# Optimization experiments

Measured on AMD Instinct MI355X. Metric: run time of the kernel, lower is better.

The kernel has to match this reference:

```python
import jax, jax.numpy as jnp
import numpy as np

B, T, D, H, L = 2, 1024, 1024, 16, 4
HD = D // H            # head_dim = 64
DFF = 4096             # 4 * d_model
VOCAB = 16384          # max_vocab_size (tied head)
MAX_CHAR = 8192        # max_char_len for RoPE table
EPS = 1e-6


def setup_inputs() -> dict:
    key = jax.random.key(0)
    ks = jax.random.split(key, 12)
    s = 0.02
    return {
        "token_ids": jax.random.randint(ks[0], (B, T), 0, 259, dtype=jnp.int32),
        "position_ids": jnp.sort(jax.random.randint(ks[1], (B, T), 0, MAX_CHAR, dtype=jnp.int32), axis=-1),
        "embed": jax.random.normal(ks[2], (VOCAB, D), jnp.float32) * s,
        "attn_norm_w": jnp.ones((L, D), jnp.float32),
        "wq": jax.random.normal(ks[3], (L, D, D), jnp.float32) * s,
        "wk": jax.random.normal(ks[4], (L, D, D), jnp.float32) * s,
        "wv": jax.random.normal(ks[5], (L, D, D), jnp.float32) * s,
        "wo": jax.random.normal(ks[6], (L, D, D), jnp.float32) * s,
        "ff_norm_w": jnp.ones((L, D), jnp.float32),
        "w1": jax.random.normal(ks[7], (L, DFF, D), jnp.float32) * s,
        "w2": jax.random.normal(ks[8], (L, D, DFF), jnp.float32) * s,
        "w3": jax.random.normal(ks[9], (L, DFF, D), jnp.float32) * s,
        "norm_w": jnp.ones((D,), jnp.float32),
    }


def _rmsnorm(x, w):
    return x * jax.lax.rsqrt(jnp.mean(x * x, axis=-1, keepdims=True) + EPS) * w


def _rope_tables():
    # precompute_freqs_cis: angles[t, i] = t / theta^(2i/dim)
    inv = 1.0 / (10000.0 ** (jnp.arange(0, HD, 2, dtype=jnp.float32) / HD))  # [HD/2]
    ang = jnp.arange(MAX_CHAR, dtype=jnp.float32)[:, None] * inv[None, :]    # [MAX_CHAR, HD/2]
    return jnp.cos(ang), jnp.sin(ang)


def _apply_rope(x, cos, sin):
    # x: [B,T,H,HD]; cos/sin: [B,T,1,HD/2] (complex multiply on (even,odd) pairs)
    xp = x.reshape(B, T, H, HD // 2, 2)
    xr, xi = xp[..., 0], xp[..., 1]
    out = jnp.stack([xr * cos - xi * sin, xr * sin + xi * cos], axis=-1)
    return out.reshape(B, T, H, HD)


def reference(token_ids, position_ids, embed, attn_norm_w, wq, wk, wv, wo,
              ff_norm_w, w1, w2, w3, norm_w):
    cos_tab, sin_tab = _rope_tables()
    cos = cos_tab[position_ids][:, :, None, :]  # [B,T,1,HD/2]
    sin = sin_tab[position_ids][:, :, None, :]

    x = embed[token_ids]  # [B,T,D] (no ghost tokens active)
    scale = 1.0 / np.sqrt(HD)

    for l in range(L):
        # --- attention block ---
        h = _rmsnorm(x, attn_norm_w[l])
        q = jnp.einsum('btd,od->bto', h, wq[l]).reshape(B, T, H, HD)
        k = jnp.einsum('btd,od->bto', h, wk[l]).reshape(B, T, H, HD)
        v = jnp.einsum('btd,od->bto', h, wv[l]).reshape(B, T, H, HD)
        q = _apply_rope(q, cos, sin)
        k = _apply_rope(k, cos, sin)
        attn = jnp.einsum('bthd,bshd->bhts', q, k) * scale  # no mask in model forward
        attn = jax.nn.softmax(attn, axis=-1)
        o = jnp.einsum('bhts,bshd->bthd', attn, v).reshape(B, T, D)
        x = x + jnp.einsum('btd,od->bto', o, wo[l])
        # --- SwiGLU FFN ---
        h = _rmsnorm(x, ff_norm_w[l])
        g = jax.nn.silu(jnp.einsum('btd,fd->btf', h, w1[l])) * jnp.einsum('btd,fd->btf', h, w3[l])
        x = x + jnp.einsum('btf,df->btd', g, w2[l])

    x = _rmsnorm(x, norm_w)
    return jnp.einsum('btd,vd->btv', x, embed)  # tied LM head -> [B,T,VOCAB]
```

## Files before the change

kernel.cpp:

```cpp
#include <hip/hip_runtime.h>

#define NTOK 2048
#define DMODEL 1024
#define NHEADS 16
#define HD_ 64
#define TSEQ 1024
#define DFF_ 4096
#define NVOCAB 16384

typedef unsigned short u16;
typedef unsigned int u32;
typedef __bf16 bf16x8 __attribute__((ext_vector_type(8)));
typedef float floatx4 __attribute__((ext_vector_type(4)));

__device__ __forceinline__ u16 f2bf(float f) {
  u32 u = __float_as_uint(f);
  u += 0x7FFFu + ((u >> 16) & 1u);
  return (u16)(u >> 16);
}
__device__ __forceinline__ float bf2f(u16 h) {
  return __uint_as_float(((u32)h) << 16);
}

__device__ __forceinline__ void gload_lds16(const void* g, void* l) {
  __builtin_amdgcn_global_load_lds(
      (const __attribute__((address_space(1))) void*)g,
      (__attribute__((address_space(3))) void*)l, 16, 0, 0);
}

__global__ void convert_bf16(const float* __restrict__ src, u16* __restrict__ dst, int n4) {
  int i = blockIdx.x * blockDim.x + threadIdx.x;
  int stride = gridDim.x * blockDim.x;
  for (; i < n4; i += stride) {
    float4 v = ((const float4*)src)[i];
    ushort4 o;
    o.x = f2bf(v.x); o.y = f2bf(v.y); o.z = f2bf(v.z); o.w = f2bf(v.w);
    ((ushort4*)dst)[i] = o;
  }
}

__global__ void convert_layer(const float* __restrict__ wq, const float* __restrict__ wk,
                              const float* __restrict__ wv, const float* __restrict__ wo,
                              const float* __restrict__ w1, const float* __restrict__ w3,
                              const float* __restrict__ w2,
                              u16* __restrict__ wqkv, u16* __restrict__ wo_b,
                              u16* __restrict__ w13, u16* __restrict__ w2_b) {
  int i = blockIdx.x * blockDim.x + threadIdx.x;
  int stride = gridDim.x * blockDim.x;
  for (; i < 4194304; i += stride) {
    const float* s; u16* d; int j;
    if (i < 262144)       { s = wq; d = wqkv;           j = i; }
    else if (i < 524288)  { s = wk; d = wqkv + 1048576; j = i - 262144; }
    else if (i < 786432)  { s = wv; d = wqkv + 2097152; j = i - 524288; }
    else if (i < 1048576) { s = wo; d = wo_b;           j = i - 786432; }
    else if (i < 2097152) { s = w1; d = w13;            j = i - 1048576; }
    else if (i < 3145728) { s = w3; d = w13 + 4194304;  j = i - 2097152; }
    else                  { s = w2; d = w2_b;           j = i - 3145728; }
    float4 v = ((const float4*)s)[j];
    ushort4 o;
    o.x = f2bf(v.x); o.y = f2bf(v.y); o.z = f2bf(v.z); o.w = f2bf(v.w);
    ((ushort4*)d)[j] = o;
  }
}

__global__ void gather_embed(const int* __restrict__ tok, const float* __restrict__ embed,
                             float* __restrict__ x) {
  int m = blockIdx.x;
  int t = tok[m];
  float4 v = ((const float4*)(embed + (long)t * DMODEL))[threadIdx.x];
  ((float4*)(x + (long)m * DMODEL))[threadIdx.x] = v;
}

__global__ void rmsnorm_bf16(const float* __restrict__ x, const float* __restrict__ w,
                             u16* __restrict__ out) {
  __shared__ float red[9];
  int m = blockIdx.x;
  int tid = threadIdx.x, lane = tid & 63, wave = tid >> 6;
  float4 v = ((const float4*)(x + (long)m * DMODEL))[tid];
  float ss = v.x * v.x + v.y * v.y + v.z * v.z + v.w * v.w;
  for (int o2 = 32; o2 > 0; o2 >>= 1) ss += __shfl_down(ss, o2);
  if (lane == 0) red[wave] = ss;
  __syncthreads();
  if (tid == 0) red[8] = rsqrtf((red[0] + red[1] + red[2] + red[3]) * (1.0f / 1024.0f) + 1e-6f);
  __syncthreads();
  float inv = red[8];
  float4 wv = ((const float4*)w)[tid];
  ushort4 o;
  o.x = f2bf(v.x * inv * wv.x); o.y = f2bf(v.y * inv * wv.y);
  o.z = f2bf(v.z * inv * wv.z); o.w = f2bf(v.w * inv * wv.w);
  ((ushort4*)(out + (long)m * DMODEL))[tid] = o;
}

__global__ void rope_qk(u16* __restrict__ qkv, const int* __restrict__ pos_ids) {
  __shared__ float cs[32], sn[32];
  int m = blockIdx.x;
  int tid = threadIdx.x;
  if (tid < 32) {
    float inv = expf(-(float)tid * (9.210340371976184f / 32.0f));
    float ang = (float)pos_ids[m] * inv;
    float s, c;
    sincosf(ang, &s, &c);
    cs[tid] = c; sn[tid] = s;
  }
  __syncthreads();
  u16* row = qkv + (long)m * 3072;
  for (int part = 0; part < 2; part++) {
    u16* base = row + part * 1024;
    for (int pp = tid; pp < 512; pp += 256) {
      int i = pp & 31;
      u32* p = (u32*)(base + pp * 2);
      u32 v = *p;
      float xr = bf2f((u16)(v & 0xFFFF));
      float xi = bf2f((u16)(v >> 16));
      float c = cs[i], s = sn[i];
      float orr = xr * c - xi * s;
      float oii = xr * s + xi * c;
      *p = (u32)f2bf(orr) | ((u32)f2bf(oii) << 16);
    }
  }
}

__global__ void transpose_v(const u16* __restrict__ qkv, u16* __restrict__ vT) {
  __shared__ u16 tile[64][65];
  int tb = blockIdx.x;
  int bh = blockIdx.y;
  int b = bh >> 4, h = bh & 15;
  const u16* src = qkv + ((long)(b * TSEQ + tb * 64)) * 3072 + 2048 + h * 64;
  for (int i = 0; i < 16; i++) {
    int e = threadIdx.x + i * 256;
    int t = e >> 6, d = e & 63;
    tile[t][d] = src[(long)t * 3072 + d];
  }
  __syncthreads();
  u16* dst = vT + ((long)bh * 64) * TSEQ + tb * 64;
  for (int i = 0; i < 16; i++) {
    int e = threadIdx.x + i * 256;
    int d = e >> 6, t = e & 63;
    dst[(long)d * TSEQ + t] = tile[t][d];
  }
}

__global__ void softmax_rows(u16* __restrict__ S) {
  __shared__ float red[9];
  long row = blockIdx.x;
  u16* p = S + row * 1024;
  int tid = threadIdx.x, lane = tid & 63, wave = tid >> 6;
  ushort4 v4 = ((const ushort4*)p)[tid];
  float v0 = bf2f(v4.x), v1 = bf2f(v4.y), v2 = bf2f(v4.z), v3 = bf2f(v4.w);
  float mx = fmaxf(fmaxf(v0, v1), fmaxf(v2, v3));
  for (int o2 = 32; o2 > 0; o2 >>= 1) mx = fmaxf(mx, __shfl_down(mx, o2));
  if (lane == 0) red[wave] = mx;
  __syncthreads();
  if (tid == 0) red[8] = fmaxf(fmaxf(red[0], red[1]), fmaxf(red[2], red[3]));
  __syncthreads();
  mx = red[8];
  float e0 = __expf(v0 - mx), e1 = __expf(v1 - mx), e2 = __expf(v2 - mx), e3 = __expf(v3 - mx);
  float s = e0 + e1 + e2 + e3;
  for (int o2 = 32; o2 > 0; o2 >>= 1) s += __shfl_down(s, o2);
  if (lane == 0) red[wave] = s;
  __syncthreads();
  if (tid == 0) red[8] = red[0] + red[1] + red[2] + red[3];
  __syncthreads();
  float inv = 1.0f / red[8];
  ushort4 o;
  o.x = f2bf(e0 * inv); o.y = f2bf(e1 * inv); o.z = f2bf(e2 * inv); o.w = f2bf(e3 * inv);
  ((ushort4*)p)[tid] = o;
}

__global__ void swiglu(const u16* __restrict__ t13, u16* __restrict__ g) {
  int i = blockIdx.x * 256 + threadIdx.x;
  int m = i >> 9, f8 = i & 511;
  const ushort4* pa = (const ushort4*)(t13 + (long)m * 8192 + f8 * 8);
  const ushort4* pb = (const ushort4*)(t13 + (long)m * 8192 + 4096 + f8 * 8);
  ushort4 a0 = pa[0], a1 = pa[1];
  ushort4 b0 = pb[0], b1 = pb[1];
  ushort4 o0, o1;
  float a, b;
#define SWG(av, bv, ov) \
  a = bf2f(av); b = bf2f(bv); ov = f2bf(a * b / (1.0f + __expf(-a)));
  SWG(a0.x, b0.x, o0.x) SWG(a0.y, b0.y, o0.y) SWG(a0.z, b0.z, o0.z) SWG(a0.w, b0.w, o0.w)
  SWG(a1.x, b1.x, o1.x) SWG(a1.y, b1.y, o1.y) SWG(a1.z, b1.z, o1.z) SWG(a1.w, b1.w, o1.w)
#undef SWG
  ushort4* po = (ushort4*)(g + (long)m * 4096 + f8 * 8);
  po[0] = o0; po[1] = o1;
}

template <int BM, int BN, int WR, int WC>
__global__ __launch_bounds__(WR * WC * 64) void gemm_nt(
    const u16* __restrict__ A, int lda, long a_sb, long a_sh,
    const u16* __restrict__ B, int ldb, long b_sb, long b_sh,
    void* __restrict__ C, int ldc, long c_sb, long c_sh,
    int K, float scale, int mode) {
  constexpr int NW = WR * WC;
  constexpr int NTHR = NW * 64;
  constexpr int WTM = BM / WR;
  constexpr int WTN = BN / WC;
  constexpr int MT = WTM / 16;
  constexpr int NT = WTN / 16;
  constexpr int ISA = (BM * 64) / (NTHR * 16);
  constexpr int ISB = (BN * 64) / (NTHR * 16);
  static_assert(ISA >= 1 && ISB >= 1, "tile too small");

  __shared__ __align__(16) u16 lA[BM * 32];
  __shared__ __align__(16) u16 lB[BN * 32];

  const int tid = threadIdx.x;
  const int lane = tid & 63;
  const int wave = tid >> 6;
  const int wm = wave / WC;
  const int wn = wave % WC;
  const int m0 = blockIdx.y * BM;
  const int n0 = blockIdx.x * BN;
  const int zb = blockIdx.z >> 4;
  const int zh = blockIdx.z & 15;
  A += (long)zb * a_sb + (long)zh * a_sh;
  B += (long)zb * b_sb + (long)zh * b_sh;
  const long c0 = (long)zb * c_sb + (long)zh * c_sh;

  floatx4 acc[MT][NT];
  for (int mi = 0; mi < MT; mi++)
    for (int ni = 0; ni < NT; ni++)
      for (int r = 0; r < 4; r++) acc[mi][ni][r] = 0.0f;

  const int q_ = lane >> 4;

  for (int k0 = 0; k0 < K; k0 += 32) {
    const u16* Ag = A + (long)m0 * lda + k0;
#pragma unroll
    for (int i = 0; i < ISA; i++) {
      int e = (tid + i * NTHR) * 8;
      int r = e >> 5;
      int c = (e >> 3) & 3;
      int csw = c ^ ((r >> 1) & 3);
      gload_lds16(Ag + (long)r * lda + (csw << 3), &lA[e]);
    }
    const u16* Bg = B + (long)n0 * ldb + k0;
#pragma unroll
    for (int i = 0; i < ISB; i++) {
      int e = (tid + i * NTHR) * 8;
      int r = e >> 5;
      int c = (e >> 3) & 3;
      int csw = c ^ ((r >> 1) & 3);
      gload_lds16(Bg + (long)r * ldb + (csw << 3), &lB[e]);
    }
    __syncthreads();

    bf16x8 af[MT], bfr[NT];
#pragma unroll
    for (int mi = 0; mi < MT; mi++) {
      int r = wm * WTM + mi * 16 + (lane & 15);
      af[mi] = *(const bf16x8*)&lA[(r << 5) + ((q_ ^ ((r >> 1) & 3)) << 3)];
    }
#pragma unroll
    for (int ni = 0; ni < NT; ni++) {
      int r = wn * WTN + ni * 16 + (lane & 15);
      bfr[ni] = *(const bf16x8*)&lB[(r << 5) + ((q_ ^ ((r >> 1) & 3)) << 3)];
    }
#pragma unroll
    for (int mi = 0; mi < MT; mi++)
#pragma unroll
      for (int ni = 0; ni < NT; ni++)
        acc[mi][ni] = __builtin_amdgcn_mfma_f32_16x16x32_bf16(af[mi], bfr[ni], acc[mi][ni], 0, 0, 0);
    __syncthreads();
  }

#pragma unroll
  for (int mi = 0; mi < MT; mi++) {
#pragma unroll
    for (int ni = 0; ni < NT; ni++) {
      int col = n0 + wn * WTN + ni * 16 + (lane & 15);
      int rbase = m0 + wm * WTM + mi * 16 + (lane >> 4) * 4;
#pragma unroll
      for (int r = 0; r < 4; r++) {
        float v = acc[mi][ni][r] * scale;
        long idx = c0 + (long)(rbase + r) * ldc + col;
        if (mode == 0)       ((float*)C)[idx] = v;
        else if (mode == 1)  ((u16*)C)[idx] = f2bf(v);
        else                 ((float*)C)[idx] += v;
      }
    }
  }
}

extern "C" void kernel_launch(void* const* d_in, const int* in_sizes, int n_in,
                              void* d_out, int out_size, void* d_ws, size_t ws_size,
                              hipStream_t stream) {
  const int*   tok         = (const int*)d_in[0];
  const int*   pos         = (const int*)d_in[1];
  const float* embed       = (const float*)d_in[2];
  const float* attn_norm_w = (const float*)d_in[3];
  const float* wq          = (const float*)d_in[4];
  const float* wk          = (const float*)d_in[5];
  const float* wv          = (const float*)d_in[6];
  const float* wo          = (const float*)d_in[7];
  const float* ff_norm_w   = (const float*)d_in[8];
  const float* w1          = (const float*)d_in[9];
  const float* w2          = (const float*)d_in[10];
  const float* w3          = (const float*)d_in[11];
  const float* norm_w      = (const float*)d_in[12];

  char* ws = (char*)d_ws;
  u16*   ebf  = (u16*)(ws);
  u16*   wqkv = (u16*)(ws + 33554432);
  u16*   wo_b = (u16*)(ws + 39845888);
  u16*   w13  = (u16*)(ws + 41943040);
  u16*   w2_b = (u16*)(ws + 58720256);
  float* x    = (float*)(ws + 67108864);
  u16*   h    = (u16*)(ws + 75497472);
  u16*   qkv  = (u16*)(ws + 79691776);
  u16*   vT   = (u16*)(ws + 92274688);
  u16*   o    = (u16*)(ws + 96468992);
  u16*   S    = (u16*)(ws + 100663296);
  u16*   t13  = S;
  u16*   g    = (u16*)(ws + 134217728);

  convert_bf16<<<16384, 256, 0, stream>>>(embed, ebf, NVOCAB * DMODEL / 4);
  gather_embed<<<NTOK, 256, 0, stream>>>(tok, embed, x);

  for (int l = 0; l < 4; l++) {
    convert_layer<<<16384, 256, 0, stream>>>(
        wq + (long)l * 1048576, wk + (long)l * 1048576, wv + (long)l * 1048576,
        wo + (long)l * 1048576, w1 + (long)l * 4194304, w3 + (long)l * 4194304,
        w2 + (long)l * 4194304, wqkv, wo_b, w13, w2_b);

    rmsnorm_bf16<<<NTOK, 256, 0, stream>>>(x, attn_norm_w + l * 1024, h);
    gemm_nt<128, 128, 2, 2><<<dim3(24, 16, 1), 256, 0, stream>>>(
        h, 1024, 0, 0, wqkv, 1024, 0, 0, qkv, 3072, 0, 0, 1024, 1.0f, 1);
    rope_qk<<<NTOK, 256, 0, stream>>>(qkv, pos);
    transpose_v<<<dim3(16, 32), 256, 0, stream>>>(qkv, vT);
    gemm_nt<128, 128, 2, 2><<<dim3(8, 8, 32), 256, 0, stream>>>(
        qkv, 3072, 3145728L, 64L,
        qkv + 1024, 3072, 3145728L, 64L,
        S, 1024, 16777216L, 1048576L, 64, 0.125f, 1);
    softmax_rows<<<32768, 256, 0, stream>>>(S);
    gemm_nt<64, 64, 2, 2><<<dim3(1, 16, 32), 256, 0, stream>>>(
        S, 1024, 16777216L, 1048576L,
        vT, 1024, 1048576L, 65536L,
        o, 1024, 1048576L, 64L, 1024, 1.0f, 1);
    gemm_nt<64, 128, 2, 2><<<dim3(8, 32, 1), 256, 0, stream>>>(
        o, 1024, 0, 0, wo_b, 1024, 0, 0, x, 1024, 0, 0, 1024, 1.0f, 2);

    rmsnorm_bf16<<<NTOK, 256, 0, stream>>>(x, ff_norm_w + l * 1024, h);
    gemm_nt<128, 128, 2, 2><<<dim3(64, 16, 1), 256, 0, stream>>>(
        h, 1024, 0, 0, w13, 1024, 0, 0, t13, 8192, 0, 0, 1024, 1.0f, 1);
    swiglu<<<4096, 256, 0, stream>>>(t13, g);
    gemm_nt<64, 128, 2, 2><<<dim3(8, 32, 1), 256, 0, stream>>>(
        g, 4096, 0, 0, w2_b, 4096, 0, 0, x, 1024, 0, 0, 4096, 1.0f, 2);
  }

  rmsnorm_bf16<<<NTOK, 256, 0, stream>>>(x, norm_w, h);
  gemm_nt<128, 128, 2, 2><<<dim3(128, 16, 1), 256, 0, stream>>>(
      h, 1024, 0, 0, ebf, 1024, 0, 0, d_out, 16384, 0, 0, 1024, 1.0f, 0);
}
```

Measured before the change: 1.640 ms.

## Add 256x256 double-buffered MFMA GEMM for FFN up-projection and LM head

Adds a new 512-thread GEMM kernel with 256x256 output tiles, swizzled LDS double buffering via direct global-to-LDS loads, explicit vmcnt waits, and s_setprio around MFMA bursts that interleave the next stage's loads. It replaces the 128x128 GEMM for the fused w1/w3 projection and the tied vocab head. The larger tiles raise arithmetic intensity and data reuse. In exchange the kernel uses 128 KB of LDS and a large accumulator set per thread, which may limit occupancy. The LM head grid of 512 blocks and the FFN grid of 256 blocks give fewer blocks to fill the CUs.

```diff
diff --git a/kernel.cpp b/kernel.cpp
--- a/kernel.cpp
+++ b/kernel.cpp
@@ -282,6 +282,165 @@
   }
 }
 
+template <int MODE>
+__global__ __launch_bounds__(512, 2) void gemm256_nt(
+    const u16* __restrict__ A, int lda,
+    const u16* __restrict__ B, int ldb,
+    void* __restrict__ C, int ldc,
+    int K, float scale) {
+  __shared__ __align__(16) u16 lA[2][16384];
+  __shared__ __align__(16) u16 lB[2][16384];
+
+  const int tid = threadIdx.x;
+  const int lane = tid & 63;
+  const int wave = tid >> 6;
+  const int wm = wave >> 2;
+  const int wn = wave & 3;
+  const int m0 = blockIdx.y * 256;
+  const int n0 = blockIdx.x * 256;
+  const int q = lane >> 4;
+  const int rl = lane & 15;
+
+  const int ck0 = ((q ^ (rl & 7)) << 3);
+  const int ck1 = (((4 | q) ^ (rl & 7)) << 3);
+  const int aRow = wm * 128 + rl;
+  const int bRow = wn * 64 + rl;
+
+  int sr[4], sc[4];
+#pragma unroll
+  for (int i = 0; i < 4; i++) {
+    int s = tid + i * 512;
+    sr[i] = s >> 3;
+    sc[i] = (((s & 7) ^ ((s >> 3) & 7)) << 3);
+  }
+
+#define STAGE256(k0, buf)                                                      \
+  {                                                                            \
+    _Pragma("unroll")                                                          \
+    for (int i = 0; i < 4; i++)                                                \
+      gload_lds16(A + (long)(m0 + sr[i]) * lda + (k0) + sc[i],                 \
+                  &lA[buf][(tid + i * 512) * 8]);                              \
+    _Pragma("unroll")                                                          \
+    for (int i = 0; i < 4; i++)                                                \
+      gload_lds16(B + (long)(n0 + sr[i]) * ldb + (k0) + sc[i],                 \
+                  &lB[buf][(tid + i * 512) * 8]);                              \
+  }
+
+  floatx4 acc[8][4];
+#pragma unroll
+  for (int mi = 0; mi < 8; mi++)
+#pragma unroll
+    for (int ni = 0; ni < 4; ni++)
+#pragma unroll
+      for (int r = 0; r < 4; r++) acc[mi][ni][r] = 0.0f;
+
+  const int NKT = K >> 6;
+  STAGE256(0, 0);
+  if (NKT > 1) {
+    STAGE256(64, 1);
+    asm volatile("s_waitcnt vmcnt(8)" ::: "memory");
+  } else {
+    asm volatile("s_waitcnt vmcnt(0)" ::: "memory");
+  }
+  __builtin_amdgcn_s_barrier();
+  __builtin_amdgcn_sched_barrier(0);
+
+  int cur = 0;
+  for (int t = 0; t < NKT; t++) {
+    const u16* pA = &lA[cur][0];
+    const u16* pB = &lB[cur][0];
+    bf16x8 aF[4][2], b01[2][2], b23[2][2];
+
+#pragma unroll
+    for (int mi = 0; mi < 4; mi++) {
+      aF[mi][0] = *(const bf16x8*)&pA[(aRow + mi * 16) * 64 + ck0];
+      aF[mi][1] = *(const bf16x8*)&pA[(aRow + mi * 16) * 64 + ck1];
+    }
+#pragma unroll
+    for (int ni = 0; ni < 2; ni++) {
+      b01[ni][0] = *(const bf16x8*)&pB[(bRow + ni * 16) * 64 + ck0];
+      b01[ni][1] = *(const bf16x8*)&pB[(bRow + ni * 16) * 64 + ck1];
+    }
+    __builtin_amdgcn_s_setprio(1);
+#pragma unroll
+    for (int mi = 0; mi < 4; mi++)
+#pragma unroll
+      for (int ni = 0; ni < 2; ni++) {
+        acc[mi][ni] = __builtin_amdgcn_mfma_f32_16x16x32_bf16(aF[mi][0], b01[ni][0], acc[mi][ni], 0, 0, 0);
+        acc[mi][ni] = __builtin_amdgcn_mfma_f32_16x16x32_bf16(aF[mi][1], b01[ni][1], acc[mi][ni], 0, 0, 0);
+      }
+    __builtin_amdgcn_s_setprio(0);
+
+#pragma unroll
+    for (int ni = 0; ni < 2; ni++) {
+      b23[ni][0] = *(const bf16x8*)&pB[(bRow + (ni + 2) * 16) * 64 + ck0];
+      b23[ni][1] = *(const bf16x8*)&pB[(bRow + (ni + 2) * 16) * 64 + ck1];
+    }
+    __builtin_amdgcn_s_setprio(1);
+#pragma unroll
+    for (int mi = 0; mi < 4; mi++)
+#pragma unroll
+      for (int ni = 0; ni < 2; ni++) {
+        acc[mi][ni + 2] = __builtin_amdgcn_mfma_f32_16x16x32_bf16(aF[mi][0], b23[ni][0], acc[mi][ni + 2], 0, 0, 0);
+        acc[mi][ni + 2] = __builtin_amdgcn_mfma_f32_16x16x32_bf16(aF[mi][1], b23[ni][1], acc[mi][ni + 2], 0, 0, 0);
+      }
+    __builtin_amdgcn_s_setprio(0);
+
+#pragma unroll
+    for (int mi = 0; mi < 4; mi++) {
+      aF[mi][0] = *(const bf16x8*)&pA[(aRow + (mi + 4) * 16) * 64 + ck0];
+      aF[mi][1] = *(const bf16x8*)&pA[(aRow + (mi + 4) * 16) * 64 + ck1];
+    }
+    __builtin_amdgcn_s_setprio(1);
+#pragma unroll
+    for (int mi = 0; mi < 4; mi++)
+#pragma unroll
+      for (int ni = 0; ni < 2; ni++) {
+        acc[mi + 4][ni + 2] = __builtin_amdgcn_mfma_f32_16x16x32_bf16(aF[mi][0], b23[ni][0], acc[mi + 4][ni + 2], 0, 0, 0);
+        acc[mi + 4][ni + 2] = __builtin_amdgcn_mfma_f32_16x16x32_bf16(aF[mi][1], b23[ni][1], acc[mi + 4][ni + 2], 0, 0, 0);
+      }
+    __builtin_amdgcn_s_setprio(0);
+    asm volatile("s_waitcnt lgkmcnt(0)" ::: "memory");
+    __builtin_amdgcn_s_barrier();
+    __builtin_amdgcn_sched_barrier(0);
+
+    if (t + 2 < NKT) STAGE256((t + 2) << 6, cur);
+    __builtin_amdgcn_s_setprio(1);
+#pragma unroll
+    for (int mi = 0; mi < 4; mi++)
+#pragma unroll
+      for (int ni = 0; ni < 2; ni++) {
+        acc[mi + 4][ni] = __builtin_amdgcn_mfma_f32_16x16x32_bf16(aF[mi][0], b01[ni][0], acc[mi + 4][ni], 0, 0, 0);
+        acc[mi + 4][ni] = __builtin_amdgcn_mfma_f32_16x16x32_bf16(aF[mi][1], b01[ni][1], acc[mi + 4][ni], 0, 0, 0);
+      }
+    __builtin_amdgcn_s_setprio(0);
+    if (t + 1 < NKT) {
+      if (t + 2 < NKT) asm volatile("s_waitcnt vmcnt(8)" ::: "memory");
+      else             asm volatile("s_waitcnt vmcnt(0)" ::: "memory");
+      __builtin_amdgcn_s_barrier();
+      __builtin_amdgcn_sched_barrier(0);
+    }
+    cur ^= 1;
+  }
+#undef STAGE256
+
+#pragma unroll
+  for (int mi = 0; mi < 8; mi++) {
+    int row = m0 + wm * 128 + mi * 16 + q * 4;
+#pragma unroll
+    for (int ni = 0; ni < 4; ni++) {
+      int col = n0 + wn * 64 + ni * 16 + rl;
+#pragma unroll
+      for (int r = 0; r < 4; r++) {
+        float v = acc[mi][ni][r] * scale;
+        long idx = (long)(row + r) * ldc + col;
+        if (MODE == 0) ((float*)C)[idx] = v;
+        else           ((u16*)C)[idx] = f2bf(v);
+      }
+    }
+  }
+}
+
 extern "C" void kernel_launch(void* const* d_in, const int* in_sizes, int n_in,
                               void* d_out, int out_size, void* d_ws, size_t ws_size,
                               hipStream_t stream) {
@@ -341,14 +500,14 @@
         o, 1024, 0, 0, wo_b, 1024, 0, 0, x, 1024, 0, 0, 1024, 1.0f, 2);
 
     rmsnorm_bf16<<<NTOK, 256, 0, stream>>>(x, ff_norm_w + l * 1024, h);
-    gemm_nt<128, 128, 2, 2><<<dim3(64, 16, 1), 256, 0, stream>>>(
-        h, 1024, 0, 0, w13, 1024, 0, 0, t13, 8192, 0, 0, 1024, 1.0f, 1);
+    gemm256_nt<1><<<dim3(32, 8, 1), 512, 0, stream>>>(
+        h, 1024, w13, 1024, t13, 8192, 1024, 1.0f);
     swiglu<<<4096, 256, 0, stream>>>(t13, g);
     gemm_nt<64, 128, 2, 2><<<dim3(8, 32, 1), 256, 0, stream>>>(
         g, 4096, 0, 0, w2_b, 4096, 0, 0, x, 1024, 0, 0, 4096, 1.0f, 2);
   }
 
   rmsnorm_bf16<<<NTOK, 256, 0, stream>>>(x, norm_w, h);
-  gemm_nt<128, 128, 2, 2><<<dim3(128, 16, 1), 256, 0, stream>>>(
-      h, 1024, 0, 0, ebf, 1024, 0, 0, d_out, 16384, 0, 0, 1024, 1.0f, 0);
-}
+  gemm256_nt<0><<<dim3(64, 8, 1), 512, 0, stream>>>(
+      h, 1024, ebf, 1024, d_out, 16384, 1024, 1.0f);
+}
```

After: 1.523 ms. 7.2% less time.
